# Kernel tuning notes

Hardware: AMD Instinct MI355X
Metric: run time of the kernel (lower is better)

## Reference

```python
import jax, jax.numpy as jnp
import numpy as np

B, S, D, H = 64, 256, 2048, 16
HD = D // H  # 128
MAXS = 256


def setup_inputs() -> dict:
    key = jax.random.key(0)
    ks = jax.random.split(key, 16)
    sc = 0.02
    inp = {
        "q": jax.random.normal(ks[0], (B, S, D), jnp.float32),
        "k": jax.random.normal(ks[1], (B, S, D), jnp.float32),
        "v": jax.random.normal(ks[2], (B, S, D), jnp.float32),
        "attention_mask": jax.random.randint(ks[3], (B, S), 0, 2, jnp.int32),
        # projection weights, torch Linear convention: y = x @ W.T + b
        "Wq": jax.random.normal(ks[4], (D, D), jnp.float32) * sc,
        "bq": jnp.zeros((D,), jnp.float32),
        "Wk": jax.random.normal(ks[5], (D, D), jnp.float32) * sc,
        "bk": jnp.zeros((D,), jnp.float32),
        "Wv": jax.random.normal(ks[6], (D, D), jnp.float32) * sc,
        "bv": jnp.zeros((D,), jnp.float32),
        "Wo": jax.random.normal(ks[7], (D, D), jnp.float32) * sc,
        "bo": jnp.zeros((D,), jnp.float32),
        # additive per-head bias table (max_sequence_length=256)
        "bias_table": jax.random.normal(ks[8], (H, MAXS, MAXS), jnp.float32) * 0.1,
    }
    return inp


def reference(q, k, v, attention_mask, Wq, bq, Wk, bk, Wv, bv, Wo, bo, bias_table):
    def proj(x, W, b):  # (B,S,D) -> (B,H,S,HD)
        y = x @ W.T + b
        return y.reshape(B, S, H, HD).transpose(0, 2, 1, 3)

    qh = proj(q, Wq, bq)
    kh = proj(k, Wk, bk)
    vh = proj(v, Wv, bv)

    # (B,H,Sq,Sk) scores
    scores = jnp.einsum("bhqd,bhkd->bhqk", qh, kh) / jnp.sqrt(jnp.float32(HD))
    scores = scores + bias_table[None, :, :S, :S]
    # mask: (B,Sk) -> (B,1,1,Sk); masked_fill where mask==0
    neg_inf = jnp.finfo(scores.dtype).min
    scores = jnp.where(attention_mask[:, None, None, :] == 0, neg_inf, scores)
    probs = jax.nn.softmax(scores, axis=-1)  # dropout p=0.0 -> identity
    out = jnp.einsum("bhqk,bhkd->bhqd", probs, vh)
    out = out.transpose(0, 2, 1, 3).reshape(B, S, D)
    return out @ Wo.T + bo
```

## Files before the change

kernel.cpp:

```cpp
#include <hip/hip_runtime.h>
#include <hip/hip_bf16.h>

typedef __attribute__((ext_vector_type(4))) float f32x4;
typedef __attribute__((ext_vector_type(8))) short s16x8;
typedef __attribute__((ext_vector_type(4))) unsigned short u16x4;
typedef __attribute__((ext_vector_type(8))) unsigned short u16x8;
typedef __attribute__((ext_vector_type(4))) int i32x4;

#define NB 64
#define NS 256
#define ND 2048
#define NH 16
#define NHD 128

__device__ __forceinline__ unsigned short f2bf(float f){
  unsigned int u = __float_as_uint(f);
  u += 0x7fffu + ((u >> 16) & 1u);
  return (unsigned short)(u >> 16);
}

__device__ __forceinline__ void gload16(const void* g, void* l){
  __builtin_amdgcn_global_load_lds(
    (const __attribute__((address_space(1))) unsigned int*)g,
    (__attribute__((address_space(3))) unsigned int*)l, 16, 0, 0);
}

#define SBAR()  __builtin_amdgcn_sched_barrier(0)
#define BARRIER() do{ SBAR(); __builtin_amdgcn_s_barrier(); SBAR(); }while(0)
#define WAIT_LGKM0() do{ asm volatile("s_waitcnt lgkmcnt(0)" ::: "memory"); SBAR(); }while(0)
#define WAIT_VM0()   do{ asm volatile("s_waitcnt vmcnt(0)"   ::: "memory"); SBAR(); }while(0)
#define WAIT_VM4()   do{ asm volatile("s_waitcnt vmcnt(4)"   ::: "memory"); SBAR(); }while(0)
#define WAIT_VM8()   do{ asm volatile("s_waitcnt vmcnt(8)"   ::: "memory"); SBAR(); }while(0)

__global__ __launch_bounds__(256) void wconv(const float* __restrict__ s,
                                             unsigned short* __restrict__ d, int n8){
  int i = blockIdx.x*256 + threadIdx.x;
  if (i >= n8) return;
  f32x4 a = *(const f32x4*)(s + (size_t)i*8);
  f32x4 b = *(const f32x4*)(s + (size_t)i*8 + 4);
  u16x8 u;
  #pragma unroll
  for (int r=0;r<4;r++){ u[r]=f2bf(a[r]); u[4+r]=f2bf(b[r]); }
  *(u16x8*)(d + (size_t)i*8) = u;
}

#define GEMM_COMMON_DECLS \
  extern __shared__ __attribute__((aligned(16))) char ldsb[]; \
  const int tid  = threadIdx.x; \
  const int lane = tid & 63, wid = tid >> 6; \
  const int g = lane >> 4, l15 = lane & 15; \
  const int wm = wid >> 2, wn = wid & 3; \
  const int nwg = gridDim.x, bid = blockIdx.x; \
  const int swz = (bid & 7) * (nwg >> 3) + (bid >> 3); \
  const int mt = swz >> 3, nt = swz & 7; \
  const int m0 = mt*256, n0 = nt*256; \
  const int srow_l = tid >> 3, slot = tid & 7;

#define RD_A(buf, qa) do{ \
    _Pragma("unroll") for (int i_=0;i_<4;i_++){ \
      int hr = (qa)*64 + i_*16 + l15; \
      const char* p_ = ldsb + (buf)*65536 + wm*16384 + hr*128; \
      _Pragma("unroll") for (int ks_=0;ks_<2;ks_++) \
        av[i_][ks_] = *(const s16x8*)(p_ + (((ks_*4+g) ^ (hr&7))*16)); } }while(0)

#define RD_B(buf, dst, qb) do{ \
    _Pragma("unroll") for (int j_=0;j_<2;j_++){ \
      int hc = (wn&1)*64 + (qb)*32 + j_*16 + l15; \
      const char* p_ = ldsb + (buf)*65536 + 32768 + (wn>>1)*16384 + hc*128; \
      _Pragma("unroll") for (int ks_=0;ks_<2;ks_++) \
        dst[j_][ks_] = *(const s16x8*)(p_ + (((ks_*4+g) ^ (hc&7))*16)); } }while(0)

#define MFMA_PH(qa, qb, bv) do{ \
    __builtin_amdgcn_s_setprio(1); \
    _Pragma("unroll") for (int i_=0;i_<4;i_++) \
      _Pragma("unroll") for (int j_=0;j_<2;j_++) \
        _Pragma("unroll") for (int ks_=0;ks_<2;ks_++) \
          acc[(qa)*4+i_][(qb)*2+j_] = __builtin_amdgcn_mfma_f32_16x16x32_bf16( \
              av[i_][ks_], bv[j_][ks_], acc[(qa)*4+i_][(qb)*2+j_], 0,0,0); \
    __builtin_amdgcn_s_setprio(0); }while(0)

#define GEMM_EPILOGUE(OUTMODE_) \
  _Pragma("unroll") \
  for (int jx=0;jx<4;jx++){ \
    int n = n0 + wn*64 + ((jx>>1)<<5) + ((jx&1)<<4) + l15; \
    float bj = bias[n]; \
    _Pragma("unroll") \
    for (int i=0;i<8;i++){ \
      int mb = m0 + wm*128 + ((i>>2)<<6) + ((i&3)<<4) + g*4; \
      if ((OUTMODE_) == 2){ \
        float* O = (float*)Out; \
        _Pragma("unroll") for (int r=0;r<4;r++) O[(size_t)(mb+r)*ND + n] = acc[i][jx][r] + bj; \
      } else if ((OUTMODE_) == 0){ \
        unsigned short* O = (unsigned short*)Out; \
        int bb = mb >> 8, h = n >> 7, d = n & 127, s0 = mb & 255; \
        _Pragma("unroll") for (int r=0;r<4;r++) \
          O[(((size_t)bb*NH + h)*NS + s0 + r)*NHD + d] = f2bf(acc[i][jx][r] + bj); \
      } else { \
        unsigned short* O = (unsigned short*)Out; \
        int bb = mb >> 8, h = n >> 7, d = n & 127, s0 = mb & 255; \
        u16x4 u; \
        _Pragma("unroll") for (int r=0;r<4;r++) u[r] = f2bf(acc[i][jx][r] + bj); \
        *(u16x4*)(O + (((size_t)bb*NH + h)*NHD + d)*NS + s0) = u; \
      } \
    } \
  }

template<int OUTMODE>
__global__ __launch_bounds__(512, 2) void gemm256(
    const unsigned short* __restrict__ A, const unsigned short* __restrict__ Bw,
    const float* __restrict__ bias, void* __restrict__ Out)
{
  GEMM_COMMON_DECLS
  const int scol = ((slot ^ (srow_l & 7)) * 8);
  const unsigned short* gsrc[4];
  gsrc[0] = A  + (size_t)(m0 +       srow_l)*ND + scol;
  gsrc[1] = A  + (size_t)(m0 + 128 + srow_l)*ND + scol;
  gsrc[2] = Bw + (size_t)(n0 +       srow_l)*ND + scol;
  gsrc[3] = Bw + (size_t)(n0 + 128 + srow_l)*ND + scol;

#define STAGE(buf, p, kt) do{ \
    const unsigned short* s_ = gsrc[p] + (kt); \
    char* d_ = ldsb + (buf)*65536 + ((p)>>1)*32768 + ((p)&1)*16384 + tid*16; \
    gload16(s_, d_); gload16(s_ + (size_t)64*ND, d_ + 8192); }while(0)

#define HALF(d, ktA, ktB, wmode) do{ \
    RD_A(d,0); RD_B(d,bva,0); \
    if ((ktA)>=0) STAGE((d)^1, 0, ktA); \
    BARRIER(); WAIT_LGKM0(); \
    MFMA_PH(0,0,bva); \
    BARRIER(); \
    RD_B(d,bvb,1); \
    if ((ktA)>=0) STAGE((d)^1, 1, ktA); \
    BARRIER(); WAIT_LGKM0(); \
    MFMA_PH(0,1,bvb); \
    BARRIER(); \
    RD_A(d,1); \
    if ((ktB)>=0) STAGE(d, 2, ktB); \
    BARRIER(); WAIT_LGKM0(); \
    MFMA_PH(1,0,bva); \
    BARRIER(); \
    if ((ktB)>=0) STAGE(d, 3, ktB); \
    MFMA_PH(1,1,bvb); \
    if ((wmode)==0){ WAIT_VM4(); BARRIER(); } \
    else if ((wmode)==1){ WAIT_VM0(); BARRIER(); } \
  }while(0)

  f32x4 acc[8][4];
  s16x8 av[4][2], bva[2][2], bvb[2][2];

  STAGE(0,0,0); STAGE(0,1,0); STAGE(0,2,0); STAGE(0,3,0);
  STAGE(1,2,64); STAGE(1,3,64);
  #pragma unroll
  for (int i=0;i<8;i++)
    #pragma unroll
    for (int j=0;j<4;j++) acc[i][j] = f32x4{0.f,0.f,0.f,0.f};
  WAIT_VM4();
  BARRIER();

  for (int t = 0; t < 15; ++t) {
    HALF(0, (2*t+1)*64, (2*t+2)*64, 0);
    HALF(1, (2*t+2)*64, (2*t+3)*64, 0);
  }
  HALF(0, 31*64, -1, 1);
  HALF(1, -1, -1, -1);

  GEMM_EPILOGUE(OUTMODE)
#undef STAGE
#undef HALF
}

template<int OUTMODE>
__global__ __launch_bounds__(512, 2) void gemm256f(
    const float* __restrict__ Af, const unsigned short* __restrict__ Bw,
    const float* __restrict__ bias, void* __restrict__ Out)
{
  GEMM_COMMON_DECLS
  const int scol = ((slot ^ (srow_l & 7)) * 8);
  const unsigned short* gsrcB[2];
  gsrcB[0] = Bw + (size_t)(n0 +       srow_l)*ND + scol;
  gsrcB[1] = Bw + (size_t)(n0 + 128 + srow_l)*ND + scol;
  const int swA = (srow_l*8 + (slot ^ (srow_l & 7)))*16;

#define STAGEB(buf, p, kt) do{ \
    const unsigned short* s_ = gsrcB[p] + (kt); \
    char* d_ = ldsb + (buf)*65536 + 32768 + (p)*16384 + tid*16; \
    gload16(s_, d_); gload16(s_ + (size_t)64*ND, d_ + 8192); }while(0)

#define STAGE_A_LOAD(p, kt, X) do{ \
    const float* s_ = Af + (size_t)(m0 + (p)*128 + srow_l)*ND + (kt) + slot*8; \
    X[0] = *(const f32x4*)(s_);               X[1] = *(const f32x4*)(s_ + 4); \
    X[2] = *(const f32x4*)(s_ + (size_t)64*ND); X[3] = *(const f32x4*)(s_ + (size_t)64*ND + 4); }while(0)

#define STAGE_A_WRITE(buf, p, X) do{ \
    u16x8 u0_, u1_; \
    _Pragma("unroll") for (int r_=0;r_<4;r_++){ \
      u0_[r_]=f2bf(X[0][r_]); u0_[4+r_]=f2bf(X[1][r_]); \
      u1_[r_]=f2bf(X[2][r_]); u1_[4+r_]=f2bf(X[3][r_]); } \
    char* w_ = ldsb + (buf)*65536 + (p)*16384 + swA; \
    *(u16x8*)(w_) = u0_; *(u16x8*)(w_ + 8192) = u1_; }while(0)

#define HALFF(d, ktA, ktB, wmode) do{ \
    RD_A(d,0); RD_B(d,bva,0); \
    if ((ktA)>=0) STAGE_A_LOAD(0, ktA, XA); \
    BARRIER(); WAIT_LGKM0(); \
    MFMA_PH(0,0,bva); \
    BARRIER(); \
    RD_B(d,bvb,1); \
    if ((ktA)>=0) STAGE_A_LOAD(1, ktA, XB); \
    BARRIER(); WAIT_LGKM0(); \
    MFMA_PH(0,1,bvb); \
    BARRIER(); \
    RD_A(d,1); \
    if ((ktB)>=0) STAGEB(d, 0, ktB); \
    BARRIER(); WAIT_LGKM0(); \
    MFMA_PH(1,0,bva); \
    BARRIER(); \
    if ((ktB)>=0) STAGEB(d, 1, ktB); \
    if ((wmode)==0) WAIT_VM4(); \
    else if ((wmode)==1) WAIT_VM0(); \
    if ((ktA)>=0){ STAGE_A_WRITE((d)^1, 0, XA); STAGE_A_WRITE((d)^1, 1, XB); } \
    MFMA_PH(1,1,bvb); \
    WAIT_LGKM0(); \
    BARRIER(); \
  }while(0)

  f32x4 acc[8][4];
  f32x4 XA[4], XB[4];
  s16x8 av[4][2], bva[2][2], bvb[2][2];

  STAGE_A_LOAD(0, 0, XA); STAGE_A_LOAD(1, 0, XB);
  STAGEB(0,0,0); STAGEB(0,1,0);
  STAGEB(1,0,64); STAGEB(1,1,64);
  #pragma unroll
  for (int i=0;i<8;i++)
    #pragma unroll
    for (int j=0;j<4;j++) acc[i][j] = f32x4{0.f,0.f,0.f,0.f};
  WAIT_VM4();
  STAGE_A_WRITE(0,0,XA); STAGE_A_WRITE(0,1,XB);
  WAIT_LGKM0();
  BARRIER();

  for (int t = 0; t < 15; ++t) {
    HALFF(0, (2*t+1)*64, (2*t+2)*64, 0);
    HALFF(1, (2*t+2)*64, (2*t+3)*64, 0);
  }
  HALFF(0, 31*64, -1, 1);
  HALFF(1, -1, -1, 2);

  GEMM_EPILOGUE(OUTMODE)
#undef STAGEB
#undef STAGE_A_LOAD
#undef STAGE_A_WRITE
#undef HALFF
}

__global__ __launch_bounds__(512, 1) void attn_fused2(
  const unsigned short* __restrict__ Qh, const unsigned short* __restrict__ Kh,
  const unsigned short* __restrict__ VT, const int* __restrict__ mask,
  const float* __restrict__ bias_table, unsigned short* __restrict__ AO)
{
  __shared__ unsigned short Klds[256*128];
  __shared__ unsigned short Vlds[128*256];
  char* Kb_ = (char*)Klds; char* Vb_ = (char*)Vlds;
  const int bh = blockIdx.x, b = bh >> 4, h = bh & 15;
  const int tid = threadIdx.x, lane = tid & 63, w = tid >> 6;
  const int g = lane >> 4, l15 = lane & 15;

  {
    const unsigned short* Ksrc = Kh + (size_t)bh*NS*NHD;
    int r0 = tid >> 4, sl = tid & 15;
    #pragma unroll
    for (int c=0;c<8;c++){
      int row = c*32 + r0;
      gload16(Ksrc + (size_t)row*NHD + ((sl ^ (row&7))*8), Kb_ + c*8192 + tid*16);
    }
  }
  {
    const unsigned short* Vsrc = VT + (size_t)bh*NHD*NS;
    int r0 = tid >> 5, sl = tid & 31;
    #pragma unroll
    for (int c=0;c<8;c++){
      int row = c*16 + r0;
      gload16(Vsrc + (size_t)row*NS + ((sl ^ (row&7))*8), Vb_ + c*8192 + tid*16);
    }
  }
  WAIT_VM8();
  BARRIER();

  const float scale = 0.08838834764831845f;
  const int* mrow = mask + b*NS;
  const int s0l = l15 + ((g&1)<<5), s1l = s0l + 16;
  const int sel = g >> 1;

  auto pass = [&](int p, bool wait_v){
    const int q = w*32 + p*16 + l15;
    const unsigned short* Qrow = Qh + ((size_t)bh*NS + q)*NHD;
    s16x8 bq[4];
    #pragma unroll
    for (int kk=0;kk<4;kk++) bq[kk] = *(const s16x8*)(Qrow + kk*32 + g*8);

    f32x4 c[16];
    __builtin_amdgcn_s_setprio(1);
    #pragma unroll
    for (int kb=0;kb<16;kb++){
      c[kb] = f32x4{0.f,0.f,0.f,0.f};
      int row = kb*16 + l15;
      #pragma unroll
      for (int kk=0;kk<4;kk++){
        s16x8 a = *(const s16x8*)(Kb_ + row*256 + (((kk*4+g) ^ (row&7))*16));
        c[kb] = __builtin_amdgcn_mfma_f32_16x16x32_bf16(a, bq[kk], c[kb], 0,0,0);
      }
    }
    __builtin_amdgcn_s_setprio(0);

    const float* brow = bias_table + ((size_t)h*NS + q)*NS;
    float mx = -3.0e38f;
    #pragma unroll
    for (int kb=0;kb<16;kb++){
      f32x4 b4 = *(const f32x4*)(brow + kb*16 + g*4);
      i32x4 m4 = *(const i32x4*)(mrow + kb*16 + g*4);
      #pragma unroll
      for (int r=0;r<4;r++){
        float val = (m4[r] != 0) ? (c[kb][r]*scale + b4[r]) : -3.0e38f;
        c[kb][r] = val;
        mx = fmaxf(mx, val);
      }
    }
    mx = fmaxf(mx, __shfl_xor(mx, 16));
    mx = fmaxf(mx, __shfl_xor(mx, 32));
    float sum = 0.f;
    #pragma unroll
    for (int kb=0;kb<16;kb++)
      #pragma unroll
      for (int r=0;r<4;r++){
        float pv = __expf(c[kb][r] - mx);
        c[kb][r] = pv; sum += pv;
      }
    sum += __shfl_xor(sum, 16);
    sum += __shfl_xor(sum, 32);
    float inv = 1.f / sum;

    unsigned int pk[16][2];
    #pragma unroll
    for (int kb=0;kb<16;kb++){
      pk[kb][0] = (unsigned int)f2bf(c[kb][0]*inv) | ((unsigned int)f2bf(c[kb][1]*inv) << 16);
      pk[kb][1] = (unsigned int)f2bf(c[kb][2]*inv) | ((unsigned int)f2bf(c[kb][3]*inv) << 16);
    }

    if (wait_v){ WAIT_VM0(); BARRIER(); }

    s16x8 pb[8];
    #pragma unroll
    for (int kk=0;kk<8;kk++){
      unsigned int e0 = (unsigned int)__shfl((int)pk[2*kk][0],   s0l);
      unsigned int e1 = (unsigned int)__shfl((int)pk[2*kk][1],   s0l);
      unsigned int e2 = (unsigned int)__shfl((int)pk[2*kk][0],   s1l);
      unsigned int e3 = (unsigned int)__shfl((int)pk[2*kk][1],   s1l);
      unsigned int o0 = (unsigned int)__shfl((int)pk[2*kk+1][0], s0l);
      unsigned int o1 = (unsigned int)__shfl((int)pk[2*kk+1][1], s0l);
      unsigned int o2 = (unsigned int)__shfl((int)pk[2*kk+1][0], s1l);
      unsigned int o3 = (unsigned int)__shfl((int)pk[2*kk+1][1], s1l);
      union { unsigned int wd[4]; s16x8 v; } u_;
      u_.wd[0] = sel ? o0 : e0; u_.wd[1] = sel ? o1 : e1;
      u_.wd[2] = sel ? o2 : e2; u_.wd[3] = sel ? o3 : e3;
      pb[kk] = u_.v;
    }

    f32x4 oacc[8];
    __builtin_amdgcn_s_setprio(1);
    #pragma unroll
    for (int dt=0;dt<8;dt++){
      oacc[dt] = f32x4{0.f,0.f,0.f,0.f};
      int row = dt*16 + l15;
      #pragma unroll
      for (int kk=0;kk<8;kk++){
        s16x8 a = *(const s16x8*)(Vb_ + row*512 + (((kk*4+g) ^ (row&7))*16));
        oacc[dt] = __builtin_amdgcn_mfma_f32_16x16x32_bf16(a, pb[kk], oacc[dt], 0,0,0);
      }
    }
    __builtin_amdgcn_s_setprio(0);

    #pragma unroll
    for (int dt=0;dt<8;dt++){
      u16x4 u;
      #pragma unroll
      for (int r=0;r<4;r++) u[r] = f2bf(oacc[dt][r]);
      *(u16x4*)(AO + ((size_t)b*NS + q)*ND + h*NHD + dt*16 + g*4) = u;
    }
  };

  pass(0, true);
  pass(1, false);
}

extern "C" void kernel_launch(void* const* d_in, const int* in_sizes, int n_in,
                              void* d_out, int out_size, void* d_ws, size_t ws_size,
                              hipStream_t stream)
{
  const float* q  = (const float*)d_in[0];
  const float* k  = (const float*)d_in[1];
  const float* v  = (const float*)d_in[2];
  const int* mask = (const int*)d_in[3];
  const float* Wq = (const float*)d_in[4];
  const float* bq = (const float*)d_in[5];
  const float* Wk = (const float*)d_in[6];
  const float* bk = (const float*)d_in[7];
  const float* Wv = (const float*)d_in[8];
  const float* bv = (const float*)d_in[9];
  const float* Wo = (const float*)d_in[10];
  const float* bo = (const float*)d_in[11];
  const float* bias_table = (const float*)d_in[12];

  char* ws = (char*)d_ws;
  unsigned short* Wqb = (unsigned short*)(ws + 0);
  unsigned short* Wkb = (unsigned short*)(ws + 8388608);
  unsigned short* Wvb = (unsigned short*)(ws + 16777216);
  unsigned short* Wob = (unsigned short*)(ws + 25165824);
  unsigned short* Qh  = (unsigned short*)(ws + 33554432);
  unsigned short* Kh  = (unsigned short*)(ws + 100663296);
  unsigned short* VT  = (unsigned short*)(ws + 167772160);
  unsigned short* AO  = (unsigned short*)(ws + 234881024);

  hipFuncSetAttribute((const void*)gemm256f<0>, hipFuncAttributeMaxDynamicSharedMemorySize, 131072);
  hipFuncSetAttribute((const void*)gemm256f<1>, hipFuncAttributeMaxDynamicSharedMemorySize, 131072);
  hipFuncSetAttribute((const void*)gemm256<2>,  hipFuncAttributeMaxDynamicSharedMemorySize, 131072);

  wconv<<<2048,256,0,stream>>>(Wq, Wqb, 524288);
  wconv<<<2048,256,0,stream>>>(Wk, Wkb, 524288);
  wconv<<<2048,256,0,stream>>>(Wv, Wvb, 524288);
  wconv<<<2048,256,0,stream>>>(Wo, Wob, 524288);

  gemm256f<0><<<512,512,131072,stream>>>(q, Wqb, bq, Qh);
  gemm256f<0><<<512,512,131072,stream>>>(k, Wkb, bk, Kh);
  gemm256f<1><<<512,512,131072,stream>>>(v, Wvb, bv, VT);

  attn_fused2<<<1024,512,0,stream>>>(Qh,Kh,VT,mask,bias_table,AO);
  gemm256<2><<<512,512,131072,stream>>>(AO,Wob,bo,(float*)d_out);
}
```

Measured before the change: 853.3 us.

## Pre-convert activations to bf16 and use bf16 GEMM for projections; trim barriers

Replaces the fp32-A projection GEMM (which converted q/k/v to bf16 inside the K loop) with a separate conversion pass into a temporary buffer followed by the pure-bf16 async-load GEMM. The four weight conversions are merged into one launch, and the bf16 GEMM drops the barrier before each LDS wait, moving the final barrier out of the wait branches. This removes register-staged fp32 loads and in-loop conversion from the GEMM, at the cost of extra activation read and write traffic and extra launches. Removing barriers risks LDS races if the remaining synchronisation is not enough.

```diff
diff --git a/kernel.cpp b/kernel.cpp
--- a/kernel.cpp
+++ b/kernel.cpp
@@ -36,6 +36,24 @@
                                              unsigned short* __restrict__ d, int n8){
   int i = blockIdx.x*256 + threadIdx.x;
   if (i >= n8) return;
+  f32x4 a = *(const f32x4*)(s + (size_t)i*8);
+  f32x4 b = *(const f32x4*)(s + (size_t)i*8 + 4);
+  u16x8 u;
+  #pragma unroll
+  for (int r=0;r<4;r++){ u[r]=f2bf(a[r]); u[4+r]=f2bf(b[r]); }
+  *(u16x8*)(d + (size_t)i*8) = u;
+}
+
+__global__ __launch_bounds__(256) void wconv4(
+  const float* __restrict__ s0, const float* __restrict__ s1,
+  const float* __restrict__ s2, const float* __restrict__ s3,
+  unsigned short* __restrict__ d0, unsigned short* __restrict__ d1,
+  unsigned short* __restrict__ d2, unsigned short* __restrict__ d3)
+{
+  int j = blockIdx.x >> 11;
+  const float* s = (j==0)?s0:(j==1)?s1:(j==2)?s2:s3;
+  unsigned short* d = (j==0)?d0:(j==1)?d1:(j==2)?d2:d3;
+  int i = (blockIdx.x & 2047)*256 + threadIdx.x;
   f32x4 a = *(const f32x4*)(s + (size_t)i*8);
   f32x4 b = *(const f32x4*)(s + (size_t)i*8 + 4);
   u16x8 u;
@@ -126,23 +144,24 @@
 #define HALF(d, ktA, ktB, wmode) do{ \
     RD_A(d,0); RD_B(d,bva,0); \
     if ((ktA)>=0) STAGE((d)^1, 0, ktA); \
-    BARRIER(); WAIT_LGKM0(); \
+    WAIT_LGKM0(); \
     MFMA_PH(0,0,bva); \
     BARRIER(); \
     RD_B(d,bvb,1); \
     if ((ktA)>=0) STAGE((d)^1, 1, ktA); \
-    BARRIER(); WAIT_LGKM0(); \
+    WAIT_LGKM0(); \
     MFMA_PH(0,1,bvb); \
     BARRIER(); \
     RD_A(d,1); \
     if ((ktB)>=0) STAGE(d, 2, ktB); \
-    BARRIER(); WAIT_LGKM0(); \
+    WAIT_LGKM0(); \
     MFMA_PH(1,0,bva); \
     BARRIER(); \
     if ((ktB)>=0) STAGE(d, 3, ktB); \
     MFMA_PH(1,1,bvb); \
-    if ((wmode)==0){ WAIT_VM4(); BARRIER(); } \
-    else if ((wmode)==1){ WAIT_VM0(); BARRIER(); } \
+    if ((wmode)==0){ WAIT_VM4(); } \
+    else if ((wmode)==1){ WAIT_VM0(); } \
+    BARRIER(); \
   }while(0)
 
   f32x4 acc[8][4];
@@ -167,91 +186,6 @@
   GEMM_EPILOGUE(OUTMODE)
 #undef STAGE
 #undef HALF
-}
-
-template<int OUTMODE>
-__global__ __launch_bounds__(512, 2) void gemm256f(
-    const float* __restrict__ Af, const unsigned short* __restrict__ Bw,
-    const float* __restrict__ bias, void* __restrict__ Out)
-{
-  GEMM_COMMON_DECLS
-  const int scol = ((slot ^ (srow_l & 7)) * 8);
-  const unsigned short* gsrcB[2];
-  gsrcB[0] = Bw + (size_t)(n0 +       srow_l)*ND + scol;
-  gsrcB[1] = Bw + (size_t)(n0 + 128 + srow_l)*ND + scol;
-  const int swA = (srow_l*8 + (slot ^ (srow_l & 7)))*16;
-
-#define STAGEB(buf, p, kt) do{ \
-    const unsigned short* s_ = gsrcB[p] + (kt); \
-    char* d_ = ldsb + (buf)*65536 + 32768 + (p)*16384 + tid*16; \
-    gload16(s_, d_); gload16(s_ + (size_t)64*ND, d_ + 8192); }while(0)
-
-#define STAGE_A_LOAD(p, kt, X) do{ \
-    const float* s_ = Af + (size_t)(m0 + (p)*128 + srow_l)*ND + (kt) + slot*8; \
-    X[0] = *(const f32x4*)(s_);               X[1] = *(const f32x4*)(s_ + 4); \
-    X[2] = *(const f32x4*)(s_ + (size_t)64*ND); X[3] = *(const f32x4*)(s_ + (size_t)64*ND + 4); }while(0)
-
-#define STAGE_A_WRITE(buf, p, X) do{ \
-    u16x8 u0_, u1_; \
-    _Pragma("unroll") for (int r_=0;r_<4;r_++){ \
-      u0_[r_]=f2bf(X[0][r_]); u0_[4+r_]=f2bf(X[1][r_]); \
-      u1_[r_]=f2bf(X[2][r_]); u1_[4+r_]=f2bf(X[3][r_]); } \
-    char* w_ = ldsb + (buf)*65536 + (p)*16384 + swA; \
-    *(u16x8*)(w_) = u0_; *(u16x8*)(w_ + 8192) = u1_; }while(0)
-
-#define HALFF(d, ktA, ktB, wmode) do{ \
-    RD_A(d,0); RD_B(d,bva,0); \
-    if ((ktA)>=0) STAGE_A_LOAD(0, ktA, XA); \
-    BARRIER(); WAIT_LGKM0(); \
-    MFMA_PH(0,0,bva); \
-    BARRIER(); \
-    RD_B(d,bvb,1); \
-    if ((ktA)>=0) STAGE_A_LOAD(1, ktA, XB); \
-    BARRIER(); WAIT_LGKM0(); \
-    MFMA_PH(0,1,bvb); \
-    BARRIER(); \
-    RD_A(d,1); \
-    if ((ktB)>=0) STAGEB(d, 0, ktB); \
-    BARRIER(); WAIT_LGKM0(); \
-    MFMA_PH(1,0,bva); \
-    BARRIER(); \
-    if ((ktB)>=0) STAGEB(d, 1, ktB); \
-    if ((wmode)==0) WAIT_VM4(); \
-    else if ((wmode)==1) WAIT_VM0(); \
-    if ((ktA)>=0){ STAGE_A_WRITE((d)^1, 0, XA); STAGE_A_WRITE((d)^1, 1, XB); } \
-    MFMA_PH(1,1,bvb); \
-    WAIT_LGKM0(); \
-    BARRIER(); \
-  }while(0)
-
-  f32x4 acc[8][4];
-  f32x4 XA[4], XB[4];
-  s16x8 av[4][2], bva[2][2], bvb[2][2];
-
-  STAGE_A_LOAD(0, 0, XA); STAGE_A_LOAD(1, 0, XB);
-  STAGEB(0,0,0); STAGEB(0,1,0);
-  STAGEB(1,0,64); STAGEB(1,1,64);
-  #pragma unroll
-  for (int i=0;i<8;i++)
-    #pragma unroll
-    for (int j=0;j<4;j++) acc[i][j] = f32x4{0.f,0.f,0.f,0.f};
-  WAIT_VM4();
-  STAGE_A_WRITE(0,0,XA); STAGE_A_WRITE(0,1,XB);
-  WAIT_LGKM0();
-  BARRIER();
-
-  for (int t = 0; t < 15; ++t) {
-    HALFF(0, (2*t+1)*64, (2*t+2)*64, 0);
-    HALFF(1, (2*t+2)*64, (2*t+3)*64, 0);
-  }
-  HALFF(0, 31*64, -1, 1);
-  HALFF(1, -1, -1, 2);
-
-  GEMM_EPILOGUE(OUTMODE)
-#undef STAGEB
-#undef STAGE_A_LOAD
-#undef STAGE_A_WRITE
-#undef HALFF
 }
 
 __global__ __launch_bounds__(512, 1) void attn_fused2(
@@ -416,23 +350,30 @@
   unsigned short* Wkb = (unsigned short*)(ws + 8388608);
   unsigned short* Wvb = (unsigned short*)(ws + 16777216);
   unsigned short* Wob = (unsigned short*)(ws + 25165824);
-  unsigned short* Qh  = (unsigned short*)(ws + 33554432);
-  unsigned short* Kh  = (unsigned short*)(ws + 100663296);
-  unsigned short* VT  = (unsigned short*)(ws + 167772160);
-  unsigned short* AO  = (unsigned short*)(ws + 234881024);
-
-  hipFuncSetAttribute((const void*)gemm256f<0>, hipFuncAttributeMaxDynamicSharedMemorySize, 131072);
-  hipFuncSetAttribute((const void*)gemm256f<1>, hipFuncAttributeMaxDynamicSharedMemorySize, 131072);
-  hipFuncSetAttribute((const void*)gemm256<2>,  hipFuncAttributeMaxDynamicSharedMemorySize, 131072);
-
-  wconv<<<2048,256,0,stream>>>(Wq, Wqb, 524288);
-  wconv<<<2048,256,0,stream>>>(Wk, Wkb, 524288);
-  wconv<<<2048,256,0,stream>>>(Wv, Wvb, 524288);
-  wconv<<<2048,256,0,stream>>>(Wo, Wob, 524288);
-
-  gemm256f<0><<<512,512,131072,stream>>>(q, Wqb, bq, Qh);
-  gemm256f<0><<<512,512,131072,stream>>>(k, Wkb, bk, Kh);
-  gemm256f<1><<<512,512,131072,stream>>>(v, Wvb, bv, VT);
+  unsigned short* tmp = (unsigned short*)(ws + 33554432);
+  unsigned short* Qh  = (unsigned short*)(ws + 100663296);
+  unsigned short* Kh  = (unsigned short*)(ws + 167772160);
+  unsigned short* VT  = (unsigned short*)(ws + 234881024);
+  unsigned short* AO  = (unsigned short*)(ws + 301989888);
+
+  hipFuncSetAttribute((const void*)gemm256<0>, hipFuncAttributeMaxDynamicSharedMemorySize, 131072);
+  hipFuncSetAttribute((const void*)gemm256<1>, hipFuncAttributeMaxDynamicSharedMemorySize, 131072);
+  hipFuncSetAttribute((const void*)gemm256<2>, hipFuncAttributeMaxDynamicSharedMemorySize, 131072);
+
+  wconv4<<<8192,256,0,stream>>>(Wq,Wk,Wv,Wo, Wqb,Wkb,Wvb,Wob);
+
+  const float* acts[3] = {q, k, v};
+  const unsigned short* wgt[3] = {Wqb, Wkb, Wvb};
+  const float* bia[3] = {bq, bk, bv};
+  unsigned short* outs[3] = {Qh, Kh, VT};
+
+  for (int x = 0; x < 3; ++x) {
+    wconv<<<16384,256,0,stream>>>(acts[x], tmp, 4194304);
+    if (x < 2)
+      gemm256<0><<<512,512,131072,stream>>>(tmp, wgt[x], bia[x], outs[x]);
+    else
+      gemm256<1><<<512,512,131072,stream>>>(tmp, wgt[x], bia[x], outs[x]);
+  }
 
   attn_fused2<<<1024,512,0,stream>>>(Qh,Kh,VT,mask,bias_table,AO);
   gemm256<2><<<512,512,131072,stream>>>(AO,Wob,bo,(float*)d_out);
```

After: 731.1 us. -14.3%, faster.
